# Performance work log

Hardware: AMD Instinct MI355X
Metric: run time of the kernel (lower is better)

Reference implementation:

```python
import jax, jax.numpy as jnp
import numpy as np

FILTER_SIZE = 3   # window length
MAJORITY = 2      # min ones per window -> at most one zero per window of 3
BIG = 1e30        # finite 'infinity' (fp32-safe)


def _segment_masks(target):
    """Precompute (from the integer target, a constant) per-timestep masks.
    Returns [T,B] float32 masks: is_zero, forced_one, dp_active, seg_start, seg_end.
    Runs of ones shorter than FILTER_SIZE are forced all-ones (len<majority, or
    len==2 with f=min(3,2)=2,m=2 -> both ones). Runs with len>=3 use the window DP."""
    t = np.asarray(target).astype(bool)
    B, T = t.shape
    prev = np.concatenate([np.zeros((B, 1), bool), t[:, :-1]], axis=1)
    nxt = np.concatenate([t[:, 1:], np.zeros((B, 1), bool)], axis=1)
    starts = t & ~prev
    ends = t & ~nxt
    idx = np.broadcast_to(np.arange(T)[None, :], (B, T))
    sidx = np.maximum.accumulate(np.where(starts, idx, -1), axis=1)
    eidx = np.minimum.accumulate(np.where(ends, idx, T)[:, ::-1], axis=1)[:, ::-1]
    run_len = np.where(t, eidx - sidx + 1, 0)
    forced = t & (run_len < FILTER_SIZE)
    dp_act = t & (run_len >= FILTER_SIZE)
    f32 = lambda a: jnp.asarray(np.ascontiguousarray(a.T), dtype=jnp.float32)
    return f32(~t), f32(forced), f32(dp_act), f32(dp_act & starts), f32(dp_act & ends)


def _median_filter_loss(c0, c1, mz, mf, ma, ms, me):
    """c0/c1: [B,T] losses vs target 0/1. Masks [T,B]. DP state = last two bits
    (index 2*prev2 + prev1); window constraint: every 3-window has >=2 ones,
    equivalently transitions: new[0]=inf; new[1]=dp[2]+c1; new[2]=dp[3]+c0;
    new[3]=min(dp[1],dp[3])+c1. Segment start resets to state (1,1) cost 0
    (ones-padding adds no extra constraints for f=3,m=2)."""
    B = c0.shape[0]
    reset = jnp.array([BIG, BIG, BIG, 0.0], c0.dtype)

    def step(carry, x):
        dp, loss = carry
        c0t, c1t, mzt, mft, mat, mst, met = x
        dpi = jnp.where(mst[:, None] > 0, reset[None, :], dp)
        n1 = dpi[:, 2] + c1t
        n2 = dpi[:, 3] + c0t
        n3 = jnp.minimum(dpi[:, 1], dpi[:, 3]) + c1t
        tr = jnp.stack([jnp.full((B,), BIG, c0t.dtype), n1, n2, n3], axis=1)
        tr = jnp.minimum(tr, BIG)
        dpn = jnp.where(mat[:, None] > 0, tr, dp)
        seg_min = jnp.min(dpn, axis=1)  # finite at segment ends (all-ones path valid)
        loss = loss + jnp.sum(mzt * c0t + mft * c1t + met * seg_min)
        return (dpn, loss), None

    xs = (c0.T, c1.T, mz, mf, ma, ms, me)
    dp0 = jnp.full((B, 4), BIG, c0.dtype).at[:, 3].set(0.0)
    (_, loss), _ = jax.lax.scan(step, (dp0, jnp.zeros((), c0.dtype)), xs)
    return loss


def setup_inputs() -> dict:
    key = jax.random.key(0)
    k1, k2 = jax.random.split(key)
    output = jax.random.normal(k1, (1024, 16384), dtype=jnp.float32)
    target = jax.random.randint(k2, (1024, 16384), 0, 2, dtype=jnp.int32)
    return {"output": output, "target": target}


def reference(output, target):
    # BCEWithLogitsLoss(reduction='none'): vs zeros -> softplus(x); vs ones -> softplus(-x)
    c0 = jax.nn.softplus(output)
    c1 = jax.nn.softplus(-output)
    mz, mf, ma, ms, me = _segment_masks(target)
    loss = _median_filter_loss(c0, c1, mz, mf, ma, ms, me)
    return loss / output.size  # reduction='mean'
```

## Files before the change

kernel.cpp:

```cpp
#include <hip/hip_runtime.h>

#define T_LEN 16384
#define K_CHUNK 32
#define BIGF 1e30f

__device__ __forceinline__ float sp0(float xv) {
    float e = __expf(-fabsf(xv));
    float l = __logf(1.0f + e);
    return fmaxf(xv, 0.0f) + l;
}

__global__ void mfl_zero(float* out) {
    if (threadIdx.x == 0) out[0] = 0.0f;
}

__global__ __launch_bounds__(256) void mfl_main(const float* __restrict__ x,
                                                const int* __restrict__ tgt,
                                                float* __restrict__ res,
                                                int total, float inv_total) {
    const int nchunks = total / K_CHUNK;
    const int stride = gridDim.x * blockDim.x;
    float acc = 0.0f;

    for (int c = blockIdx.x * blockDim.x + threadIdx.x; c < nchunks; c += stride) {
        const int p0 = c * K_CHUNK;
        const int trow = p0 & (T_LEN - 1);

        float xs[32];
        unsigned m = 0;
        const float4* xp = (const float4*)(x + p0);
        const int4*  tp = (const int4*)(tgt + p0);
        #pragma unroll
        for (int j = 0; j < 8; j++) {
            float4 v = xp[j];
            xs[4*j+0] = v.x; xs[4*j+1] = v.y; xs[4*j+2] = v.z; xs[4*j+3] = v.w;
        }
        #pragma unroll
        for (int j = 0; j < 8; j++) {
            int4 t = tp[j];
            m |= (unsigned)(t.x != 0) << (4*j+0);
            m |= (unsigned)(t.y != 0) << (4*j+1);
            m |= (unsigned)(t.z != 0) << (4*j+2);
            m |= (unsigned)(t.w != 0) << (4*j+3);
        }

        const int pl = (p0 + K_CHUNK + 8 <= total) ? (p0 + K_CHUNK) : p0;
        float la[8];
        unsigned lm = 0;
        {
            const float4* lxp = (const float4*)(x + pl);
            const int4*  ltp = (const int4*)(tgt + pl);
            float4 a0 = lxp[0], a1 = lxp[1];
            int4   b0 = ltp[0], b1 = ltp[1];
            la[0]=a0.x; la[1]=a0.y; la[2]=a0.z; la[3]=a0.w;
            la[4]=a1.x; la[5]=a1.y; la[6]=a1.z; la[7]=a1.w;
            lm  = (unsigned)(b0.x!=0)      | ((unsigned)(b0.y!=0)<<1)
                | ((unsigned)(b0.z!=0)<<2) | ((unsigned)(b0.w!=0)<<3)
                | ((unsigned)(b1.x!=0)<<4) | ((unsigned)(b1.y!=0)<<5)
                | ((unsigned)(b1.z!=0)<<6) | ((unsigned)(b1.w!=0)<<7);
        }

        unsigned amask = 0xFFFFFFFFu;
        if (trow != 0 && tgt[p0 - 1] != 0) {
            unsigned nm = ~m;
            amask = (nm == 0u) ? 0u : (0xFFFFFFFFu << __builtin_ctz(nm));
        }
        const unsigned mm = m & amask;
        const unsigned ss = mm & ~(mm << 1);
        const unsigned hm = (~mm) & (mm << 1);

        float v1 = BIGF, v2 = BIGF, v3 = 0.0f, s1 = 0.0f;
        int leni = 0;
        #pragma unroll
        for (int i = 0; i < 32; i++) {
            const float xv = xs[i];
            acc += sp0(xv);
            const bool harvf = (hm >> i) & 1u;
            const float hv = (leni < 3) ? s1 : fminf(v1, fminf(v2, v3));
            acc += harvf ? hv : 0.0f;
            const bool startf = (ss >> i) & 1u;
            const float r1 = startf ? BIGF : v1;
            const float r2 = startf ? BIGF : v2;
            const float r3 = startf ? 0.0f : v3;
            const float s1r = startf ? 0.0f : s1;
            const int   lr  = startf ? 0    : leni;
            v1 = r2 - xv;
            v2 = r3;
            v3 = fminf(r1, r3) - xv;
            s1 = s1r - xv;
            leni = lr + 1;
        }

        if ((mm >> 31) & 1u) {
            if (trow + K_CHUNK < T_LEN) {
                const unsigned g = lm & 0xFFu;
                const int k = (g == 0xFFu) ? 8 : (int)__builtin_ctz(~g & 0xFFu);
                #pragma unroll
                for (int j = 0; j < 8; j++) {
                    if (j < k) {
                        const float xv = la[j];
                        const float n1 = v2 - xv;
                        const float n2 = v3;
                        const float n3 = fminf(v1, v3) - xv;
                        v1 = n1; v2 = n2; v3 = n3;
                        s1 -= xv; leni++;
                    }
                }
                if (k == 8) {
                    int t = trow + K_CHUNK + 8, pp = p0 + K_CHUNK + 8;
                    while (t < T_LEN) {
                        const int4   tq = *(const int4*)(tgt + pp);
                        const float4 xq = *(const float4*)(x + pp);
                        const unsigned g4 = (unsigned)(tq.x != 0)
                                          | ((unsigned)(tq.y != 0) << 1)
                                          | ((unsigned)(tq.z != 0) << 2)
                                          | ((unsigned)(tq.w != 0) << 3);
                        const int k4 = (g4 == 0xFu) ? 4 : (int)__builtin_ctz(~g4 & 0xFu);
                        const float xv4[4] = {xq.x, xq.y, xq.z, xq.w};
                        #pragma unroll
                        for (int j = 0; j < 4; j++) {
                            if (j < k4) {
                                const float xv = xv4[j];
                                const float n1 = v2 - xv;
                                const float n2 = v3;
                                const float n3 = fminf(v1, v3) - xv;
                                v1 = n1; v2 = n2; v3 = n3;
                                s1 -= xv; leni++;
                            }
                        }
                        if (k4 < 4) break;
                        t += 4; pp += 4;
                    }
                }
            }
            acc += (leni < 3) ? s1 : fminf(v1, fminf(v2, v3));
        }
    }

    #pragma unroll
    for (int off = 32; off > 0; off >>= 1)
        acc += __shfl_down(acc, off);

    __shared__ float smem[4];
    const int lane = threadIdx.x & 63;
    const int wid = threadIdx.x >> 6;
    if (lane == 0) smem[wid] = acc;
    __syncthreads();
    if (threadIdx.x == 0) {
        float b = (smem[0] + smem[1]) + (smem[2] + smem[3]);
        atomicAdd(res, b * inv_total);
    }
}

extern "C" void kernel_launch(void* const* d_in, const int* in_sizes, int n_in,
                              void* d_out, int out_size, void* d_ws, size_t ws_size,
                              hipStream_t stream) {
    const float* x = (const float*)d_in[0];
    const int* tgt = (const int*)d_in[1];
    float* res = (float*)d_out;
    const int total = in_sizes[0];

    mfl_zero<<<1, 64, 0, stream>>>(res);

    const int threads = 256;
    const int nchunks = total / K_CHUNK;
    const int blocks = (nchunks + threads - 1) / threads;
    mfl_main<<<blocks, threads, 0, stream>>>(x, tgt, res, total,
                                             1.0f / (float)total);
}
```

Measured before the change: 155.4 us.

## Double chunk size to 64 and precompute short-run harvest mask

Each thread now processes 64 timesteps per chunk using 64-bit masks, which halves the number of chunks and the overhead of boundary lookahead, prefix checks and run continuation per element. The per-step run-length counter is replaced by a precomputed bitmask that marks short runs, and the final run length is derived from a count-leading-zeros. The softplus sum is split across two accumulators to shorten the dependency chain. Larger chunks raise register pressure (64 floats held per thread) and cut the thread count, which may lower occupancy and weaken latency hiding.

```diff
diff --git a/kernel.cpp b/kernel.cpp
--- a/kernel.cpp
+++ b/kernel.cpp
@@ -1,8 +1,9 @@
 #include <hip/hip_runtime.h>
 
 #define T_LEN 16384
-#define K_CHUNK 32
+#define K_CHUNK 64
 #define BIGF 1e30f
+typedef unsigned long long u64;
 
 __device__ __forceinline__ float sp0(float xv) {
     float e = __expf(-fabsf(xv));
@@ -20,28 +21,28 @@
                                                 int total, float inv_total) {
     const int nchunks = total / K_CHUNK;
     const int stride = gridDim.x * blockDim.x;
-    float acc = 0.0f;
+    float acc0 = 0.0f, acc0b = 0.0f, acc1 = 0.0f;
 
     for (int c = blockIdx.x * blockDim.x + threadIdx.x; c < nchunks; c += stride) {
         const int p0 = c * K_CHUNK;
         const int trow = p0 & (T_LEN - 1);
 
-        float xs[32];
-        unsigned m = 0;
+        float xs[64];
+        u64 m = 0;
         const float4* xp = (const float4*)(x + p0);
         const int4*  tp = (const int4*)(tgt + p0);
         #pragma unroll
-        for (int j = 0; j < 8; j++) {
+        for (int j = 0; j < 16; j++) {
             float4 v = xp[j];
             xs[4*j+0] = v.x; xs[4*j+1] = v.y; xs[4*j+2] = v.z; xs[4*j+3] = v.w;
         }
         #pragma unroll
-        for (int j = 0; j < 8; j++) {
+        for (int j = 0; j < 16; j++) {
             int4 t = tp[j];
-            m |= (unsigned)(t.x != 0) << (4*j+0);
-            m |= (unsigned)(t.y != 0) << (4*j+1);
-            m |= (unsigned)(t.z != 0) << (4*j+2);
-            m |= (unsigned)(t.w != 0) << (4*j+3);
+            m |= (u64)(t.x != 0) << (4*j+0);
+            m |= (u64)(t.y != 0) << (4*j+1);
+            m |= (u64)(t.z != 0) << (4*j+2);
+            m |= (u64)(t.w != 0) << (4*j+3);
         }
 
         const int pl = (p0 + K_CHUNK + 8 <= total) ? (p0 + K_CHUNK) : p0;
@@ -60,38 +61,41 @@
                 | ((unsigned)(b1.z!=0)<<6) | ((unsigned)(b1.w!=0)<<7);
         }
 
-        unsigned amask = 0xFFFFFFFFu;
+        u64 amask = ~0ull;
         if (trow != 0 && tgt[p0 - 1] != 0) {
-            unsigned nm = ~m;
-            amask = (nm == 0u) ? 0u : (0xFFFFFFFFu << __builtin_ctz(nm));
+            u64 nm = ~m;
+            amask = (nm == 0ull) ? 0ull : (~0ull << __builtin_ctzll(nm));
         }
-        const unsigned mm = m & amask;
-        const unsigned ss = mm & ~(mm << 1);
-        const unsigned hm = (~mm) & (mm << 1);
+        const u64 mm = m & amask;
+        const u64 ss = mm & ~(mm << 1);
+        const u64 hm = (~mm) & (mm << 1);
+        const u64 sh = hm & ((ss << 1) | (ss << 2));
 
         float v1 = BIGF, v2 = BIGF, v3 = 0.0f, s1 = 0.0f;
-        int leni = 0;
         #pragma unroll
-        for (int i = 0; i < 32; i++) {
+        for (int i = 0; i < 64; i++) {
             const float xv = xs[i];
-            acc += sp0(xv);
-            const bool harvf = (hm >> i) & 1u;
-            const float hv = (leni < 3) ? s1 : fminf(v1, fminf(v2, v3));
-            acc += harvf ? hv : 0.0f;
-            const bool startf = (ss >> i) & 1u;
+            const float sp = sp0(xv);
+            if (i & 1) acc0b += sp; else acc0 += sp;
+            const bool harvf  = (hm >> i) & 1ull;
+            const bool shortf = (sh >> i) & 1ull;
+            const float m3 = fminf(v1, fminf(v2, v3));
+            const float hv = shortf ? s1 : m3;
+            acc1 += harvf ? hv : 0.0f;
+            const bool startf = (ss >> i) & 1ull;
             const float r1 = startf ? BIGF : v1;
             const float r2 = startf ? BIGF : v2;
             const float r3 = startf ? 0.0f : v3;
             const float s1r = startf ? 0.0f : s1;
-            const int   lr  = startf ? 0    : leni;
             v1 = r2 - xv;
             v2 = r3;
             v3 = fminf(r1, r3) - xv;
             s1 = s1r - xv;
-            leni = lr + 1;
         }
 
-        if ((mm >> 31) & 1u) {
+        if ((mm >> 63) & 1ull) {
+            const u64 nmm = ~mm;
+            int leni = (nmm == 0ull) ? 64 : (int)__builtin_clzll(nmm);
             if (trow + K_CHUNK < T_LEN) {
                 const unsigned g = lm & 0xFFu;
                 const int k = (g == 0xFFu) ? 8 : (int)__builtin_ctz(~g & 0xFFu);
@@ -133,9 +137,11 @@
                     }
                 }
             }
-            acc += (leni < 3) ? s1 : fminf(v1, fminf(v2, v3));
+            acc1 += (leni < 3) ? s1 : fminf(v1, fminf(v2, v3));
         }
     }
+
+    float acc = (acc0 + acc0b) + acc1;
 
     #pragma unroll
     for (int off = 32; off > 0; off >>= 1)
```

New measurement: 159.8 us. 1.03x slower.
